# Kernel tuning notes

Hardware: AMD Instinct MI355X
Metric: run time of the kernel (lower is better)

Reference implementation:

```python
import jax, jax.numpy as jnp
import numpy as np

# geometry constants from init_kwargs
VX, VY, VZ = 0.1, 0.1, 4.0
X_OFF, Y_OFF, Z_OFF = VX / 2 - 51.2, VY / 2 - 51.2, VZ / 2 - 3.0
GY, GX = 1024, 1024  # round((51.2-(-51.2))/0.1)
NUM_BEV = 8
BN_EPS = 1e-3


def setup_inputs() -> dict:
    key = jax.random.key(0)
    k1, k2, k3, k4, k5, k6 = jax.random.split(key, 6)
    N, P, C_in, C_out = 40000, 32, 10, 64
    voxel_features = jax.random.normal(k1, (N, P, 4), jnp.float32)
    voxel_num_points = jax.random.randint(k2, (N,), 1, P + 1, jnp.int32)
    bb = jax.random.randint(k3, (N,), 0, 2, jnp.int32)
    yy = jax.random.randint(k4, (N,), 0, GY, jnp.int32)
    xx = jax.random.randint(k5, (N,), 0, GX, jnp.int32)
    coords = jnp.stack([bb, jnp.zeros((N,), jnp.int32), yy, xx], axis=1)
    record_len = jnp.array([N // 2, N - N // 2], jnp.int32)
    W = jax.random.normal(k6, (C_in, C_out), jnp.float32) * 0.1
    gamma = jnp.ones((C_out,), jnp.float32)
    beta = jnp.zeros((C_out,), jnp.float32)
    run_mean = jnp.zeros((C_out,), jnp.float32)
    run_var = jnp.ones((C_out,), jnp.float32)
    return {"voxel_features": voxel_features, "W": W, "gamma": gamma,
            "beta": beta, "run_mean": run_mean, "run_var": run_var,
            "voxel_num_points": voxel_num_points, "coords": coords,
            "record_len": record_len}


def reference(voxel_features, W, gamma, beta, run_mean, run_var,
              voxel_num_points, coords, record_len):
    N, P, _ = voxel_features.shape
    npts = voxel_num_points.astype(voxel_features.dtype)  # [N]
    xyz = voxel_features[:, :, :3]

    # cluster offset feature
    points_mean = xyz.sum(axis=1, keepdims=True) / npts[:, None, None]
    f_cluster = xyz - points_mean

    # pillar-center offset feature
    cx = coords[:, 3].astype(voxel_features.dtype)[:, None] * VX + X_OFF
    cy = coords[:, 2].astype(voxel_features.dtype)[:, None] * VY + Y_OFF
    cz = coords[:, 1].astype(voxel_features.dtype)[:, None] * VZ + Z_OFF
    f_center = jnp.stack([xyz[:, :, 0] - cx, xyz[:, :, 1] - cy,
                          xyz[:, :, 2] - cz], axis=-1)

    features = jnp.concatenate([voxel_features, f_cluster, f_center], axis=-1)  # [N,P,10]

    # padding mask
    mask = (voxel_num_points[:, None] > jnp.arange(P, dtype=jnp.int32)[None, :])
    mask = mask[..., None].astype(voxel_features.dtype)  # [N,P,1]
    features = features * mask

    # PFN layer: Linear(10->64, no bias) + BN(eval) + ReLU + max over points
    x = jnp.einsum('npc,cd->npd', features, W)  # [N,P,64]
    x = (x - run_mean) * jax.lax.rsqrt(run_var + BN_EPS) * gamma + beta
    x = jax.nn.relu(x)
    pillar_features = x.max(axis=1)  # [N,64]

    # hand-crafted BEV stats
    safe_n = jnp.clip(npts, 1.0)[:, None]  # [N,1]
    num_points_norm = npts[:, None] / P
    intensity = voxel_features[:, :, 3:4]
    mean_intensity = (intensity * mask).sum(axis=1) / safe_n
    z = xyz[:, :, 2:3]
    mean_height = (z * mask).sum(axis=1) / safe_n
    max_height = (z * mask + (1 - mask) * -1e6).max(axis=1)
    min_height = (z * mask + (1 - mask) * 1e6).min(axis=1)
    height_span = max_height - min_height
    pm = (xyz * mask).sum(axis=1, keepdims=True) / safe_n[:, :, None]
    var_xyz = (((xyz - pm) ** 2) * mask).sum(axis=1) / safe_n  # [N,3]
    pillar_bev = jnp.concatenate([num_points_norm, mean_intensity, mean_height,
                                  max_height, height_span, var_xyz[:, 0:1],
                                  var_xyz[:, 1:2], var_xyz[:, 2:3]], axis=1)  # [N,8]

    batch_size = record_len.shape[0]
    b = jnp.clip(coords[:, 0], 0, batch_size - 1)
    y_idx = coords[:, 2]
    x_idx = coords[:, 3]
    vox_bev = jnp.zeros((batch_size, NUM_BEV, GY, GX), voxel_features.dtype)
    vox_bev = vox_bev.at[b, :, y_idx, x_idx].set(pillar_bev)

    return pillar_features, vox_bev
```

## Files before the change

### kernel.cpp

```cpp
#include <hip/hip_runtime.h>

#define GYD 1024
#define GXD 1024
#define NUM_BEV 8

__device__ __forceinline__ float bcast0(float x) {
    return __int_as_float(__builtin_amdgcn_readfirstlane(__float_as_int(x)));
}
__device__ __forceinline__ float rsum32(float x) {
#pragma unroll
    for (int o = 1; o < 32; o <<= 1) x += __shfl_xor(x, o, 64);
    return x;
}
__device__ __forceinline__ float rmax32(float x) {
#pragma unroll
    for (int o = 1; o < 32; o <<= 1) x = fmaxf(x, __shfl_xor(x, o, 64));
    return x;
}
__device__ __forceinline__ float rmin32(float x) {
#pragma unroll
    for (int o = 1; o < 32; o <<= 1) x = fminf(x, __shfl_xor(x, o, 64));
    return x;
}

__global__ __launch_bounds__(256) void pillar_kernel(
    const float4* __restrict__ vf,
    const float* __restrict__ W,
    const float* __restrict__ gammap, const float* __restrict__ betap,
    const float* __restrict__ rmean, const float* __restrict__ rvar,
    const int* __restrict__ npts_arr,
    const int* __restrict__ coords,
    float* __restrict__ pillar_out,
    float* __restrict__ bev_vals,
    int* __restrict__ winner,
    int N, int bs)
{
    __shared__ float4 pts[4][32];
    const int wid  = threadIdx.x >> 6;
    const int lane = threadIdx.x & 63;
    const int n    = blockIdx.x * 4 + wid;
    const bool valid = (n < N);
    const int nn = valid ? n : 0;

    const int d = lane;
    const float w0 = W[d],        w1 = W[64 + d],  w2 = W[128 + d], w3 = W[192 + d];
    const float w4 = W[256 + d],  w5 = W[320 + d], w6 = W[384 + d];
    const float w7 = W[448 + d],  w8 = W[512 + d], w9 = W[576 + d];
    const float g  = gammap[d], bt = betap[d], rm = rmean[d], rv = rvar[d];

    const int npts = npts_arr[nn];
    const int cb   = coords[nn * 4 + 0];
    const int czi  = coords[nn * 4 + 1];
    const int cyi  = coords[nn * 4 + 2];
    const int cxi  = coords[nn * 4 + 3];
    const float cx = (float)cxi * 0.1f - 51.15f;
    const float cy = (float)cyi * 0.1f - 51.15f;
    const float cz = (float)czi * 4.0f - 1.0f;

    float4 v = make_float4(0.f, 0.f, 0.f, 0.f);
    bool pv = false;
    if (valid && lane < 32) {
        v = vf[(size_t)nn * 32 + lane];
        pv = (lane < npts);
    }
    float4 v0;
    v0.x = __shfl(v.x, 0, 64); v0.y = __shfl(v.y, 0, 64);
    v0.z = __shfl(v.z, 0, 64); v0.w = __shfl(v.w, 0, 64);
    if (valid && lane < 32) pts[wid][lane] = pv ? v : v0;

    const float m    = pv ? 1.f : 0.f;
    const float fn   = (float)npts;
    const float invn = 1.f / fn;

    const float sx   = rsum32(v.x);
    const float sy   = rsum32(v.y);
    const float sz   = rsum32(v.z);
    const float smx  = rsum32(v.x * m);
    const float smy  = rsum32(v.y * m);
    const float smz  = rsum32(v.z * m);
    const float smI  = rsum32(v.w * m);
    const float sx2  = rsum32(v.x * v.x * m);
    const float sy2  = rsum32(v.y * v.y * m);
    const float sz2  = rsum32(v.z * v.z * m);
    const float maxz = rmax32(pv ? v.z : -1e6f);
    const float minz = rmin32(pv ? v.z :  1e6f);

    const float mx_ = bcast0(sx) * invn;
    const float my_ = bcast0(sy) * invn;
    const float mz_ = bcast0(sz) * invn;

    __syncthreads();

    const float scale = g * rsqrtf(rv + 1e-3f);
    const float shift = bt - rm * scale;
    const float A = (w0 + w4 + w7) * scale;
    const float B = (w1 + w5 + w8) * scale;
    const float C = (w2 + w6 + w9) * scale;
    const float D = w3 * scale;
    const float E = -(mx_ * w4 + my_ * w5 + mz_ * w6 + cx * w7 + cy * w8 + cz * w9);
    const float base = fmaf(E, scale, shift);

    float a0 = -1e30f, a1 = -1e30f, a2 = -1e30f, a3 = -1e30f;
#pragma unroll
    for (int p = 0; p < 32; p += 4) {
        const float4 q0 = pts[wid][p + 0];
        const float4 q1 = pts[wid][p + 1];
        const float4 q2 = pts[wid][p + 2];
        const float4 q3 = pts[wid][p + 3];
        a0 = fmaxf(a0, fmaf(q0.x, A, fmaf(q0.y, B, fmaf(q0.z, C, fmaf(q0.w, D, base)))));
        a1 = fmaxf(a1, fmaf(q1.x, A, fmaf(q1.y, B, fmaf(q1.z, C, fmaf(q1.w, D, base)))));
        a2 = fmaxf(a2, fmaf(q2.x, A, fmaf(q2.y, B, fmaf(q2.z, C, fmaf(q2.w, D, base)))));
        a3 = fmaxf(a3, fmaf(q3.x, A, fmaf(q3.y, B, fmaf(q3.z, C, fmaf(q3.w, D, base)))));
    }
    float acc = fmaxf(fmaxf(a0, a1), fmaxf(a2, a3));
    if (npts < 32) acc = fmaxf(acc, shift);
    acc = fmaxf(acc, 0.f);

    if (valid) {
        pillar_out[(size_t)n * 64 + lane] = acc;
        if (lane == 0) {
            const float pmx = smx * invn, pmy = smy * invn, pmz = smz * invn;
            const float vvx = fmaf(-pmx, pmx, sx2 * invn);
            const float vvy = fmaf(-pmy, pmy, sy2 * invn);
            const float vvz = fmaf(-pmz, pmz, sz2 * invn);
            float4* bvp = (float4*)&bev_vals[(size_t)n * 8];
            bvp[0] = make_float4(fn * (1.f / 32.f), smI * invn, pmz, maxz);
            bvp[1] = make_float4(maxz - minz, vvx, vvy, vvz);
            int b = cb < 0 ? 0 : (cb > bs - 1 ? bs - 1 : cb);
            const int cell = (b * GYD + cyi) * GXD + cxi;
            atomicMax(&winner[cell], n + 1);
        }
    }
}

__global__ __launch_bounds__(256) void scatter_kernel(
    const int* __restrict__ coords,
    const float* __restrict__ bev_vals,
    const int* __restrict__ winner,
    float* __restrict__ vox_bev,
    int N, int bs)
{
    const int t = blockIdx.x * blockDim.x + threadIdx.x;
    const int n = t >> 3, k = t & 7;
    if (n >= N) return;
    const int cb = coords[n * 4 + 0];
    const int y  = coords[n * 4 + 2];
    const int x  = coords[n * 4 + 3];
    const int b  = cb < 0 ? 0 : (cb > bs - 1 ? bs - 1 : cb);
    const int cell = (b * GYD + y) * GXD + x;
    if (winner[cell] == n + 1)
        vox_bev[(((size_t)b * NUM_BEV + k) * GYD + y) * GXD + x] = bev_vals[(size_t)n * 8 + k];
}

extern "C" void kernel_launch(void* const* d_in, const int* in_sizes, int n_in,
                              void* d_out, int out_size, void* d_ws, size_t ws_size,
                              hipStream_t stream) {
    const float4* vf    = (const float4*)d_in[0];
    const float* W      = (const float*)d_in[1];
    const float* gammap = (const float*)d_in[2];
    const float* betap  = (const float*)d_in[3];
    const float* rmean  = (const float*)d_in[4];
    const float* rvar   = (const float*)d_in[5];
    const int* npts     = (const int*)d_in[6];
    const int* coords   = (const int*)d_in[7];
    const int N  = in_sizes[6];
    const int bs = in_sizes[8];

    float* pillar_out = (float*)d_out;
    float* vox_bev    = (float*)d_out + (size_t)N * 64;

    int* winner     = (int*)d_ws;
    float* bev_vals = (float*)((char*)d_ws + (size_t)bs * GYD * GXD * sizeof(int));

    hipMemsetAsync(winner, 0, (size_t)bs * GYD * GXD * sizeof(int), stream);
    hipMemsetAsync(vox_bev, 0, (size_t)bs * NUM_BEV * GYD * GXD * sizeof(float), stream);

    const int blocksA = (N + 3) / 4;
    pillar_kernel<<<blocksA, 256, 0, stream>>>(vf, W, gammap, betap, rmean, rvar,
                                               npts, coords, pillar_out, bev_vals,
                                               winner, N, bs);
    const int blocksB = (N * NUM_BEV + 255) / 256;
    scatter_kernel<<<blocksB, 256, 0, stream>>>(coords, bev_vals, winner, vox_bev, N, bs);
}
```

Measured before the change: 156.7 us.

## Pack two pillars per wavefront and replace BEV memset+scatter with dense fill

Each 64-lane wavefront now handles two pillars, one per 32-lane half, so the point loads and reductions use every lane instead of leaving half the lanes idle. The separate memset of the 64 MB BEV output and the sparse scatter kernel are replaced by a dense fill kernel. It reads the winner index for each cell and writes all 8 channels, either the gathered stats or zeros. The output is written once instead of memset then scatter, at the cost of reading the 8 MB winner array densely.

Result: faster. 135.9 us (-13.3%).

```diff
diff --git a/kernel.cpp b/kernel.cpp
--- a/kernel.cpp
+++ b/kernel.cpp
@@ -4,8 +4,8 @@
 #define GXD 1024
 #define NUM_BEV 8
 
-__device__ __forceinline__ float bcast0(float x) {
-    return __int_as_float(__builtin_amdgcn_readfirstlane(__float_as_int(x)));
+__device__ __forceinline__ float rdlane(float x, int l) {
+    return __int_as_float(__builtin_amdgcn_readlane(__float_as_int(x), l));
 }
 __device__ __forceinline__ float rsum32(float x) {
 #pragma unroll
@@ -27,7 +27,7 @@
     const float4* __restrict__ vf,
     const float* __restrict__ W,
     const float* __restrict__ gammap, const float* __restrict__ betap,
-    const float* __restrict__ rmean, const float* __restrict__ rvar,
+    const float* __restrict__ rmeanp, const float* __restrict__ rvarp,
     const int* __restrict__ npts_arr,
     const int* __restrict__ coords,
     float* __restrict__ pillar_out,
@@ -35,43 +35,38 @@
     int* __restrict__ winner,
     int N, int bs)
 {
-    __shared__ float4 pts[4][32];
+    __shared__ float4 pts[4][2][32];
     const int wid  = threadIdx.x >> 6;
     const int lane = threadIdx.x & 63;
-    const int n    = blockIdx.x * 4 + wid;
+    const int half = lane >> 5;
+    const int sl   = lane & 31;
+    const int n0   = blockIdx.x * 8 + wid * 2;
+    const int n    = n0 + half;
     const bool valid = (n < N);
     const int nn = valid ? n : 0;
 
     const int d = lane;
-    const float w0 = W[d],        w1 = W[64 + d],  w2 = W[128 + d], w3 = W[192 + d];
-    const float w4 = W[256 + d],  w5 = W[320 + d], w6 = W[384 + d];
-    const float w7 = W[448 + d],  w8 = W[512 + d], w9 = W[576 + d];
-    const float g  = gammap[d], bt = betap[d], rm = rmean[d], rv = rvar[d];
+    const float w0 = W[d],       w1 = W[64 + d],  w2 = W[128 + d], w3 = W[192 + d];
+    const float w4 = W[256 + d], w5 = W[320 + d], w6 = W[384 + d];
+    const float w7 = W[448 + d], w8 = W[512 + d], w9 = W[576 + d];
+    const float g  = gammap[d], bt = betap[d], rm = rmeanp[d], rv = rvarp[d];
 
     const int npts = npts_arr[nn];
-    const int cb   = coords[nn * 4 + 0];
-    const int czi  = coords[nn * 4 + 1];
-    const int cyi  = coords[nn * 4 + 2];
-    const int cxi  = coords[nn * 4 + 3];
-    const float cx = (float)cxi * 0.1f - 51.15f;
-    const float cy = (float)cyi * 0.1f - 51.15f;
-    const float cz = (float)czi * 4.0f - 1.0f;
+    const int4 crd = ((const int4*)coords)[nn];
+    const float cx = (float)crd.w * 0.1f - 51.15f;
+    const float cy = (float)crd.z * 0.1f - 51.15f;
+    const float cz = (float)crd.y * 4.0f - 1.0f;
 
     float4 v = make_float4(0.f, 0.f, 0.f, 0.f);
-    bool pv = false;
-    if (valid && lane < 32) {
-        v = vf[(size_t)nn * 32 + lane];
-        pv = (lane < npts);
-    }
+    if (valid) v = vf[(size_t)nn * 32 + sl];
+    const bool pv = sl < npts;
+    const int src = half << 5;
     float4 v0;
-    v0.x = __shfl(v.x, 0, 64); v0.y = __shfl(v.y, 0, 64);
-    v0.z = __shfl(v.z, 0, 64); v0.w = __shfl(v.w, 0, 64);
-    if (valid && lane < 32) pts[wid][lane] = pv ? v : v0;
+    v0.x = __shfl(v.x, src, 64); v0.y = __shfl(v.y, src, 64);
+    v0.z = __shfl(v.z, src, 64); v0.w = __shfl(v.w, src, 64);
+    pts[wid][half][sl] = pv ? v : v0;
 
-    const float m    = pv ? 1.f : 0.f;
-    const float fn   = (float)npts;
-    const float invn = 1.f / fn;
-
+    const float m = pv ? 1.f : 0.f;
     const float sx   = rsum32(v.x);
     const float sy   = rsum32(v.y);
     const float sz   = rsum32(v.z);
@@ -85,71 +80,77 @@
     const float maxz = rmax32(pv ? v.z : -1e6f);
     const float minz = rmin32(pv ? v.z :  1e6f);
 
-    const float mx_ = bcast0(sx) * invn;
-    const float my_ = bcast0(sy) * invn;
-    const float mz_ = bcast0(sz) * invn;
-
     __syncthreads();
 
     const float scale = g * rsqrtf(rv + 1e-3f);
-    const float shift = bt - rm * scale;
+    const float shift = fmaf(-rm, scale, bt);
     const float A = (w0 + w4 + w7) * scale;
     const float B = (w1 + w5 + w8) * scale;
     const float C = (w2 + w6 + w9) * scale;
     const float D = w3 * scale;
-    const float E = -(mx_ * w4 + my_ * w5 + mz_ * w6 + cx * w7 + cy * w8 + cz * w9);
-    const float base = fmaf(E, scale, shift);
 
-    float a0 = -1e30f, a1 = -1e30f, a2 = -1e30f, a3 = -1e30f;
 #pragma unroll
-    for (int p = 0; p < 32; p += 4) {
-        const float4 q0 = pts[wid][p + 0];
-        const float4 q1 = pts[wid][p + 1];
-        const float4 q2 = pts[wid][p + 2];
-        const float4 q3 = pts[wid][p + 3];
-        a0 = fmaxf(a0, fmaf(q0.x, A, fmaf(q0.y, B, fmaf(q0.z, C, fmaf(q0.w, D, base)))));
-        a1 = fmaxf(a1, fmaf(q1.x, A, fmaf(q1.y, B, fmaf(q1.z, C, fmaf(q1.w, D, base)))));
-        a2 = fmaxf(a2, fmaf(q2.x, A, fmaf(q2.y, B, fmaf(q2.z, C, fmaf(q2.w, D, base)))));
-        a3 = fmaxf(a3, fmaf(q3.x, A, fmaf(q3.y, B, fmaf(q3.z, C, fmaf(q3.w, D, base)))));
+    for (int h = 0; h < 2; ++h) {
+        const int L  = h << 5;
+        const int nh = __builtin_amdgcn_readlane(npts, L);
+        const float invnh = 1.f / (float)nh;
+        const float mx = rdlane(sx, L) * invnh, my = rdlane(sy, L) * invnh, mz = rdlane(sz, L) * invnh;
+        const float cxh = rdlane(cx, L), cyh = rdlane(cy, L), czh = rdlane(cz, L);
+        const float E   = -(mx * w4 + my * w5 + mz * w6 + cxh * w7 + cyh * w8 + czh * w9);
+        const float bse = fmaf(E, scale, shift);
+
+        float a0 = -1e30f, a1 = -1e30f, a2 = -1e30f, a3 = -1e30f;
+#pragma unroll
+        for (int p = 0; p < 32; p += 4) {
+            const float4 q0 = pts[wid][h][p + 0];
+            const float4 q1 = pts[wid][h][p + 1];
+            const float4 q2 = pts[wid][h][p + 2];
+            const float4 q3 = pts[wid][h][p + 3];
+            a0 = fmaxf(a0, fmaf(q0.x, A, fmaf(q0.y, B, fmaf(q0.z, C, fmaf(q0.w, D, bse)))));
+            a1 = fmaxf(a1, fmaf(q1.x, A, fmaf(q1.y, B, fmaf(q1.z, C, fmaf(q1.w, D, bse)))));
+            a2 = fmaxf(a2, fmaf(q2.x, A, fmaf(q2.y, B, fmaf(q2.z, C, fmaf(q2.w, D, bse)))));
+            a3 = fmaxf(a3, fmaf(q3.x, A, fmaf(q3.y, B, fmaf(q3.z, C, fmaf(q3.w, D, bse)))));
+        }
+        float acc = fmaxf(fmaxf(a0, a1), fmaxf(a2, a3));
+        if (nh < 32) acc = fmaxf(acc, shift);
+        acc = fmaxf(acc, 0.f);
+        const int np_ = n0 + h;
+        if (np_ < N) pillar_out[(size_t)np_ * 64 + lane] = acc;
     }
-    float acc = fmaxf(fmaxf(a0, a1), fmaxf(a2, a3));
-    if (npts < 32) acc = fmaxf(acc, shift);
-    acc = fmaxf(acc, 0.f);
 
-    if (valid) {
-        pillar_out[(size_t)n * 64 + lane] = acc;
-        if (lane == 0) {
-            const float pmx = smx * invn, pmy = smy * invn, pmz = smz * invn;
-            const float vvx = fmaf(-pmx, pmx, sx2 * invn);
-            const float vvy = fmaf(-pmy, pmy, sy2 * invn);
-            const float vvz = fmaf(-pmz, pmz, sz2 * invn);
-            float4* bvp = (float4*)&bev_vals[(size_t)n * 8];
-            bvp[0] = make_float4(fn * (1.f / 32.f), smI * invn, pmz, maxz);
-            bvp[1] = make_float4(maxz - minz, vvx, vvy, vvz);
-            int b = cb < 0 ? 0 : (cb > bs - 1 ? bs - 1 : cb);
-            const int cell = (b * GYD + cyi) * GXD + cxi;
-            atomicMax(&winner[cell], n + 1);
-        }
+    if (valid && sl == 0) {
+        const float fn = (float)npts, invn = 1.f / fn;
+        const float pmx = smx * invn, pmy = smy * invn, pmz = smz * invn;
+        const float vvx = fmaf(-pmx, pmx, sx2 * invn);
+        const float vvy = fmaf(-pmy, pmy, sy2 * invn);
+        const float vvz = fmaf(-pmz, pmz, sz2 * invn);
+        float4* bvp = (float4*)&bev_vals[(size_t)n * 8];
+        bvp[0] = make_float4(fn * (1.f / 32.f), smI * invn, pmz, maxz);
+        bvp[1] = make_float4(maxz - minz, vvx, vvy, vvz);
+        const int b = crd.x < 0 ? 0 : (crd.x > bs - 1 ? bs - 1 : crd.x);
+        atomicMax(&winner[(b * GYD + crd.z) * GXD + crd.w], n + 1);
     }
 }
 
-__global__ __launch_bounds__(256) void scatter_kernel(
-    const int* __restrict__ coords,
+__global__ __launch_bounds__(256) void bev_fill(
+    const int* __restrict__ winner,
     const float* __restrict__ bev_vals,
-    const int* __restrict__ winner,
-    float* __restrict__ vox_bev,
-    int N, int bs)
+    float* __restrict__ vox_bev, int bs)
 {
-    const int t = blockIdx.x * blockDim.x + threadIdx.x;
-    const int n = t >> 3, k = t & 7;
-    if (n >= N) return;
-    const int cb = coords[n * 4 + 0];
-    const int y  = coords[n * 4 + 2];
-    const int x  = coords[n * 4 + 3];
-    const int b  = cb < 0 ? 0 : (cb > bs - 1 ? bs - 1 : cb);
-    const int cell = (b * GYD + y) * GXD + x;
-    if (winner[cell] == n + 1)
-        vox_bev[(((size_t)b * NUM_BEV + k) * GYD + y) * GXD + x] = bev_vals[(size_t)n * 8 + k];
+    const int cell = blockIdx.x * 256 + threadIdx.x;
+    const int w = winner[cell];
+    float4 lo = make_float4(0.f, 0.f, 0.f, 0.f), hi = lo;
+    if (w > 0) {
+        const float4* bvp = (const float4*)&bev_vals[(size_t)(w - 1) * 8];
+        lo = bvp[0]; hi = bvp[1];
+    }
+    const int b  = cell >> 20;
+    const int yx = cell & ((1 << 20) - 1);
+    float* basep = vox_bev + (((size_t)b * NUM_BEV) << 20) + yx;
+    basep[(size_t)0 << 20] = lo.x; basep[(size_t)1 << 20] = lo.y;
+    basep[(size_t)2 << 20] = lo.z; basep[(size_t)3 << 20] = lo.w;
+    basep[(size_t)4 << 20] = hi.x; basep[(size_t)5 << 20] = hi.y;
+    basep[(size_t)6 << 20] = hi.z; basep[(size_t)7 << 20] = hi.w;
 }
 
 extern "C" void kernel_launch(void* const* d_in, const int* in_sizes, int n_in,
@@ -159,8 +160,8 @@
     const float* W      = (const float*)d_in[1];
     const float* gammap = (const float*)d_in[2];
     const float* betap  = (const float*)d_in[3];
-    const float* rmean  = (const float*)d_in[4];
-    const float* rvar   = (const float*)d_in[5];
+    const float* rmeanp = (const float*)d_in[4];
+    const float* rvarp  = (const float*)d_in[5];
     const int* npts     = (const int*)d_in[6];
     const int* coords   = (const int*)d_in[7];
     const int N  = in_sizes[6];
@@ -173,12 +174,11 @@
     float* bev_vals = (float*)((char*)d_ws + (size_t)bs * GYD * GXD * sizeof(int));
 
     hipMemsetAsync(winner, 0, (size_t)bs * GYD * GXD * sizeof(int), stream);
-    hipMemsetAsync(vox_bev, 0, (size_t)bs * NUM_BEV * GYD * GXD * sizeof(float), stream);
 
-    const int blocksA = (N + 3) / 4;
-    pillar_kernel<<<blocksA, 256, 0, stream>>>(vf, W, gammap, betap, rmean, rvar,
+    const int blocksA = (N + 7) / 8;
+    pillar_kernel<<<blocksA, 256, 0, stream>>>(vf, W, gammap, betap, rmeanp, rvarp,
                                                npts, coords, pillar_out, bev_vals,
                                                winner, N, bs);
-    const int blocksB = (N * NUM_BEV + 255) / 256;
-    scatter_kernel<<<blocksB, 256, 0, stream>>>(coords, bev_vals, winner, vox_bev, N, bs);
+    const int blocksB = (bs << 20) / 256;
+    bev_fill<<<blocksB, 256, 0, stream>>>(winner, bev_vals, vox_bev, bs);
 }
```
